# Optimization experiments

Hardware: AMD Instinct MI355X
Metric: run time of the kernel (lower is better)

## Reference

```python
import jax, jax.numpy as jnp
import numpy as np
import math

B, S, D, H = 1, 4096, 1024, 16
DH = D // H


def setup_inputs() -> dict:
    key = jax.random.key(0)
    k1, k2, k3 = jax.random.split(key, 3)
    x = jax.random.normal(k1, (B, S, D), dtype=jnp.float32)
    # additive causal mask: 0 where allowed, -1e9 where masked (future)
    causal = jnp.tril(jnp.ones((S, S), dtype=bool))
    mask = jnp.where(causal, 0.0, -1e9).astype(jnp.float32)[None]  # [1,S,S]
    W_attn = jax.random.normal(k2, (D, 3 * D), dtype=jnp.float32) * 0.02
    b_attn = jnp.zeros((3 * D,), dtype=jnp.float32)
    W_proj = jax.random.normal(k3, (D, D), dtype=jnp.float32) * 0.02
    b_proj = jnp.zeros((D,), dtype=jnp.float32)
    return {"x": x, "mask": mask, "W_attn": W_attn, "b_attn": b_attn,
            "W_proj": W_proj, "b_proj": b_proj}


def reference(x, mask, W_attn, b_attn, W_proj, b_proj):
    # c_attn: fused QKV projection
    qkv = x @ W_attn + b_attn                      # [B,S,3D]
    q, k, v = jnp.split(qkv, 3, axis=-1)           # each [B,S,D]

    def heads(t):  # [B,S,D] -> [B,H,S,DH]
        return t.reshape(B, S, H, DH).transpose(0, 2, 1, 3)

    q, k, v = heads(q), heads(k), heads(v)
    # scores: eager O(S^2) matrix as in original
    w = jnp.einsum('bhqd,bhkd->bhqk', q, k) / math.sqrt(DH)
    w = w + mask[:, None, :, :]                    # broadcast over heads
    w = jax.nn.softmax(w, axis=-1)                 # dropout p=0 -> identity
    a = jnp.einsum('bhqk,bhkd->bhqd', w, v)        # [B,H,S,DH]
    a = a.transpose(0, 2, 1, 3).reshape(B, S, D)   # merge heads
    return a @ W_proj + b_proj
```

## Files before the change

### kernel.cpp

```cpp
#include <hip/hip_runtime.h>

typedef _Float16 half8 __attribute__((ext_vector_type(8)));
typedef short short8 __attribute__((ext_vector_type(8)));
typedef float floatx4 __attribute__((ext_vector_type(4)));

static __device__ __forceinline__ float bf2f(unsigned short u) {
  union { unsigned int u; float f; } c; c.u = ((unsigned int)u) << 16; return c.f;
}
static __device__ __forceinline__ unsigned short f2bf(float f) {
  union { float f; unsigned int u; } c; c.f = f;
  return (unsigned short)((c.u + 0x7fffu + ((c.u >> 16) & 1u)) >> 16);
}

#define GL2LDS16(gsrc, ldst)                                                        \
  __builtin_amdgcn_global_load_lds(                                                 \
      (const __attribute__((address_space(1))) void*)(const void*)(gsrc),           \
      (__attribute__((address_space(3))) void*)(void*)(ldst), 16, 0, 0)

static __device__ __forceinline__ int dtype_bf16(const unsigned short* mask16) {
  return mask16[1] != 0;
}

__global__ __launch_bounds__(256) void k_prep(const void* __restrict__ x,
    const void* __restrict__ Wa, const void* __restrict__ Wp,
    const unsigned short* __restrict__ mask16, _Float16* __restrict__ xh,
    _Float16* __restrict__ WaT, _Float16* __restrict__ WpT) {
  __shared__ float tile[32][33];
  const int dt = dtype_bf16(mask16);
  const int bx = blockIdx.x;
  if (bx < 4096) {
    const int i = (bx * 256 + threadIdx.x) * 4;
    _Float16 o[4];
    if (dt) {
      ushort4 u = *((const ushort4*)((const unsigned short*)x + i));
      o[0] = (_Float16)bf2f(u.x); o[1] = (_Float16)bf2f(u.y);
      o[2] = (_Float16)bf2f(u.z); o[3] = (_Float16)bf2f(u.w);
    } else {
      float4 f = *((const float4*)((const float*)x + i));
      o[0] = (_Float16)f.x; o[1] = (_Float16)f.y;
      o[2] = (_Float16)f.z; o[3] = (_Float16)f.w;
    }
    union { _Float16 h[4]; uint2 u; } pk;
    pk.h[0] = o[0]; pk.h[1] = o[1]; pk.h[2] = o[2]; pk.h[3] = o[3];
    *((uint2*)(xh + i)) = pk.u;
    return;
  }
  const void* in; _Float16* out; int n0, k0;
  if (bx < 7168) { const int b = bx - 4096; in = Wa; out = WaT;
                   n0 = (b % 96) * 32; k0 = (b / 96) * 32;
    const int N = 3072, tid = threadIdx.x, c = tid & 31, r0 = tid >> 5;
#pragma unroll
    for (int i = 0; i < 4; ++i) {
      const int r = r0 + i * 8;
      const size_t src = (size_t)(k0 + r) * N + (n0 + c);
      tile[r][c] = dt ? bf2f(((const unsigned short*)in)[src]) : ((const float*)in)[src];
    }
  } else { const int b = bx - 7168; in = Wp; out = WpT;
           n0 = (b % 32) * 32; k0 = (b / 32) * 32;
    const int N = 1024, tid = threadIdx.x, c = tid & 31, r0 = tid >> 5;
#pragma unroll
    for (int i = 0; i < 4; ++i) {
      const int r = r0 + i * 8;
      const size_t src = (size_t)(k0 + r) * N + (n0 + c);
      tile[r][c] = dt ? bf2f(((const unsigned short*)in)[src]) : ((const float*)in)[src];
    }
  }
  __syncthreads();
  const int tid = threadIdx.x, c = tid & 31, r0 = tid >> 5;
#pragma unroll
  for (int i = 0; i < 4; ++i) {
    const int rr = r0 + i * 8;
    out[(size_t)(n0 + rr) * 1024 + (k0 + c)] = (_Float16)tile[c][rr];
  }
}

template <int KD>
static __device__ __forceinline__ void gemm_mainloop(const _Float16* __restrict__ A,
    const _Float16* __restrict__ Bt, int m0, int n0,
    _Float16* As, _Float16* Bs, floatx4 acc[4][4]) {
  const int tid = threadIdx.x;
  const int wave = tid >> 6, lane = tid & 63;
  const int lq = lane & 15, quad = lane >> 4;
  const int wm = (wave >> 1) * 64, wn = (wave & 1) * 64;
  const int scol = (lane & 3) * 8;
  for (int k0 = 0; k0 < KD; k0 += 32) {
    __syncthreads();
#pragma unroll
    for (int op = 0; op < 2; ++op) {
      const int rbase = wave * 32 + op * 16;
      const int row = rbase + (lane >> 2);
      GL2LDS16(A + (size_t)(m0 + row) * KD + k0 + scol, As + rbase * 32);
      GL2LDS16(Bt + (size_t)(n0 + row) * KD + k0 + scol, Bs + rbase * 32);
    }
    __builtin_amdgcn_s_waitcnt(0x0f70);
    __syncthreads();
    half8 af[4], bf[4];
#pragma unroll
    for (int i = 0; i < 4; ++i) {
      af[i] = *(const half8*)(As + (wm + i * 16 + lq) * 32 + quad * 8);
      bf[i] = *(const half8*)(Bs + (wn + i * 16 + lq) * 32 + quad * 8);
    }
#pragma unroll
    for (int i = 0; i < 4; ++i)
#pragma unroll
      for (int j = 0; j < 4; ++j)
        acc[i][j] = __builtin_amdgcn_mfma_f32_16x16x32_f16(af[i], bf[j], acc[i][j], 0, 0, 0);
  }
}

__global__ __launch_bounds__(256, 1) void k_gemm_qkv(const _Float16* __restrict__ A,
    const _Float16* __restrict__ Bt, const void* __restrict__ bias,
    const unsigned short* __restrict__ mask16, _Float16* __restrict__ Qb,
    _Float16* __restrict__ Kb, unsigned short* __restrict__ VTb) {
  __shared__ __attribute__((aligned(16))) _Float16 As[128 * 32];
  __shared__ __attribute__((aligned(16))) _Float16 Bs[128 * 32];
  const int tid = threadIdx.x, wave = tid >> 6, lane = tid & 63;
  const int lq = lane & 15, quad = lane >> 4;
  const int m0 = blockIdx.y * 128, n0 = blockIdx.x * 128;
  const int wm = (wave >> 1) * 64, wn = (wave & 1) * 64;
  floatx4 acc[4][4] = {};
  gemm_mainloop<1024>(A, Bt, m0, n0, As, Bs, acc);
  const int dt = dtype_bf16(mask16);
  const int sec = n0 >> 10;
  const float scale = (sec == 0) ? 0.1803368801f : 1.0f;
#pragma unroll
  for (int i = 0; i < 4; ++i) {
    const int growb = m0 + wm + i * 16 + quad * 4;
#pragma unroll
    for (int j = 0; j < 4; ++j) {
      const int gcol = n0 + wn + j * 16 + lq;
      const int c = gcol & 1023, hh = c >> 6, dh = c & 63;
      const float bv = dt ? bf2f(((const unsigned short*)bias)[gcol])
                          : ((const float*)bias)[gcol];
      if (sec == 2) {
        union { unsigned short u[4]; uint2 v; } pk;
#pragma unroll
        for (int r = 0; r < 4; ++r) pk.u[r] = f2bf(acc[i][j][r] + bv);
        *(uint2*)(VTb + (size_t)(hh * 64 + dh) * 4096 + growb) = pk.v;
      } else {
        _Float16* dst = (sec == 0) ? Qb : Kb;
#pragma unroll
        for (int r = 0; r < 4; ++r)
          dst[(size_t)(hh * 4096 + growb + r) * 64 + dh] =
              (_Float16)((acc[i][j][r] + bv) * scale);
      }
    }
  }
}

__global__ __launch_bounds__(256, 3) void k_attn(const _Float16* __restrict__ Qb,
    const _Float16* __restrict__ Kb, const unsigned short* __restrict__ VTb,
    unsigned short* __restrict__ Op0, unsigned short* __restrict__ Op1,
    float* __restrict__ Lp) {
  constexpr int S = 4096;
  const int bx = blockIdx.x;
  const int half = bx >> 9;
  const int i5 = bx & 511;
  const int h = i5 & 15;
  const int idx = i5 >> 4;
  const int qb = half ? idx : (31 - idx);
  const int q0 = qb * 128;
  const int t0 = half * (qb + 1);
  const int t1 = t0 + qb + 1;
  const int tid = threadIdx.x, wave = tid >> 6, lane = tid & 63;
  const int lq = lane & 15, quad = lane >> 4;
  __shared__ __attribute__((aligned(16))) _Float16 Ks[64 * 72];
  __shared__ __attribute__((aligned(16))) unsigned short VTs[64 * 72];
  __shared__ __attribute__((aligned(16))) unsigned short Ps[4][32 * 72];
  const _Float16* Qh = Qb + (size_t)h * S * 64;
  const _Float16* Kh = Kb + (size_t)h * S * 64;
  const unsigned short* VTh = VTb + (size_t)h * 64 * S;
  const int qw = q0 + wave * 32;
  half8 qf[2][2];
#pragma unroll
  for (int m = 0; m < 2; ++m)
#pragma unroll
    for (int c = 0; c < 2; ++c)
      qf[m][c] = *(const half8*)(Qh + (size_t)(qw + m * 16 + lq) * 64 + c * 32 + quad * 8);
  short8 aones;
#pragma unroll
  for (int jj = 0; jj < 8; ++jj) aones[jj] = (short)0x3F80;
  floatx4 o[4][2] = {};
  floatx4 ol[2] = {};
  const int srow = tid >> 2, schunk = (tid & 3) * 16;
  uint4 kreg0, kreg1, vreg0, vreg1;
  {
    const int kt = t0 * 64;
    kreg0 = *(const uint4*)(Kh + (size_t)(kt + srow) * 64 + schunk);
    kreg1 = *(const uint4*)(Kh + (size_t)(kt + srow) * 64 + schunk + 8);
    vreg0 = *(const uint4*)(VTh + (size_t)srow * S + kt + schunk);
    vreg1 = *(const uint4*)(VTh + (size_t)srow * S + kt + schunk + 8);
  }
  unsigned short* Pw = &Ps[wave][0];
  for (int t = t0; t < t1; ++t) {
    const int kt = t * 64;
    __syncthreads();
    *(uint4*)(Ks + srow * 72 + schunk) = kreg0;
    *(uint4*)(Ks + srow * 72 + schunk + 8) = kreg1;
    *(uint4*)(VTs + srow * 72 + schunk) = vreg0;
    *(uint4*)(VTs + srow * 72 + schunk + 8) = vreg1;
    __syncthreads();
    if (t + 1 < t1) {
      const int kn = kt + 64;
      kreg0 = *(const uint4*)(Kh + (size_t)(kn + srow) * 64 + schunk);
      kreg1 = *(const uint4*)(Kh + (size_t)(kn + srow) * 64 + schunk + 8);
      vreg0 = *(const uint4*)(VTh + (size_t)srow * S + kn + schunk);
      vreg1 = *(const uint4*)(VTh + (size_t)srow * S + kn + schunk + 8);
    }
    floatx4 sc[2][4];
    {
      half8 kf0[4], kf1[4];
#pragma unroll
      for (int nf = 0; nf < 4; ++nf) {
        kf0[nf] = *(const half8*)(Ks + (nf * 16 + lq) * 72 + quad * 8);
        kf1[nf] = *(const half8*)(Ks + (nf * 16 + lq) * 72 + 32 + quad * 8);
      }
#pragma unroll
      for (int m = 0; m < 2; ++m)
#pragma unroll
        for (int nf = 0; nf < 4; ++nf) {
          floatx4 z = {0.f, 0.f, 0.f, 0.f};
          z = __builtin_amdgcn_mfma_f32_16x16x32_f16(kf0[nf], qf[m][0], z, 0, 0, 0);
          sc[m][nf] = __builtin_amdgcn_mfma_f32_16x16x32_f16(kf1[nf], qf[m][1], z, 0, 0, 0);
        }
    }
#pragma unroll
    for (int m = 0; m < 2; ++m) {
      const int q = qw + m * 16 + lq;
      if (kt + 63 > qw + m * 16) {
#pragma unroll
        for (int nf = 0; nf < 4; ++nf) {
          const int key = kt + nf * 16 + quad * 4;
          float p[4];
#pragma unroll
          for (int r = 0; r < 4; ++r) {
            float e = __builtin_amdgcn_exp2f(sc[m][nf][r]);
            p[r] = (key + r > q) ? 0.f : e;
          }
          uint2 pk;
          pk.x = __builtin_amdgcn_perm(__float_as_uint(p[1]), __float_as_uint(p[0]),
                                       0x07060302u);
          pk.y = __builtin_amdgcn_perm(__float_as_uint(p[3]), __float_as_uint(p[2]),
                                       0x07060302u);
          *(uint2*)(Pw + (m * 16 + lq) * 72 + nf * 16 + quad * 4) = pk;
        }
      } else {
#pragma unroll
        for (int nf = 0; nf < 4; ++nf) {
          float p[4];
#pragma unroll
          for (int r = 0; r < 4; ++r) p[r] = __builtin_amdgcn_exp2f(sc[m][nf][r]);
          uint2 pk;
          pk.x = __builtin_amdgcn_perm(__float_as_uint(p[1]), __float_as_uint(p[0]),
                                       0x07060302u);
          pk.y = __builtin_amdgcn_perm(__float_as_uint(p[3]), __float_as_uint(p[2]),
                                       0x07060302u);
          *(uint2*)(Pw + (m * 16 + lq) * 72 + nf * 16 + quad * 4) = pk;
        }
      }
    }
    __builtin_amdgcn_s_waitcnt(0xC07F);
#pragma unroll
    for (int c = 0; c < 2; ++c) {
      short8 pf[2];
#pragma unroll
      for (int m = 0; m < 2; ++m)
        pf[m] = *(const short8*)(Pw + (m * 16 + lq) * 72 + c * 32 + quad * 8);
#pragma unroll
      for (int nf = 0; nf < 4; ++nf) {
        const short8 vfr = *(const short8*)(VTs + (nf * 16 + lq) * 72 + c * 32 + quad * 8);
#pragma unroll
        for (int m = 0; m < 2; ++m)
          o[nf][m] = __builtin_amdgcn_mfma_f32_16x16x32_bf16(vfr, pf[m], o[nf][m], 0, 0, 0);
      }
#pragma unroll
      for (int m = 0; m < 2; ++m)
        ol[m] = __builtin_amdgcn_mfma_f32_16x16x32_bf16(aones, pf[m], ol[m], 0, 0, 0);
    }
  }
  unsigned short* Op = half ? Op1 : Op0;
#pragma unroll
  for (int m = 0; m < 2; ++m) {
    const int q = qw + m * 16 + lq;
#pragma unroll
    for (int nf = 0; nf < 4; ++nf) {
      union { unsigned short u[4]; uint2 v; } pk;
#pragma unroll
      for (int r = 0; r < 4; ++r) pk.u[r] = f2bf(o[nf][m][r]);
      *(uint2*)(Op + (size_t)q * 1024 + h * 64 + nf * 16 + quad * 4) = pk.v;
    }
    if (quad == 0) Lp[half * 65536 + h * 4096 + q] = ol[m][0];
  }
}

__global__ __launch_bounds__(256) void k_merge(const unsigned short* __restrict__ Op0,
    const unsigned short* __restrict__ Op1, const float* __restrict__ Lp,
    _Float16* __restrict__ Ah) {
  const int row = blockIdx.x;
  const int c = threadIdx.x * 4;
  const int h = c >> 6;
  const float l = Lp[h * 4096 + row] + Lp[65536 + h * 4096 + row];
  const float inv = __builtin_amdgcn_rcpf(l);
  const size_t idx = (size_t)row * 1024 + c;
  const ushort4 a = *(const ushort4*)(Op0 + idx);
  const ushort4 b = *(const ushort4*)(Op1 + idx);
  union { _Float16 h4[4]; uint2 u; } pk;
  pk.h4[0] = (_Float16)((bf2f(a.x) + bf2f(b.x)) * inv);
  pk.h4[1] = (_Float16)((bf2f(a.y) + bf2f(b.y)) * inv);
  pk.h4[2] = (_Float16)((bf2f(a.z) + bf2f(b.z)) * inv);
  pk.h4[3] = (_Float16)((bf2f(a.w) + bf2f(b.w)) * inv);
  *(uint2*)(Ah + idx) = pk.u;
}

__global__ __launch_bounds__(256, 1) void k_gemm_proj(const _Float16* __restrict__ A,
    const _Float16* __restrict__ Bt, const void* __restrict__ bias,
    const unsigned short* __restrict__ mask16, void* __restrict__ out) {
  __shared__ __attribute__((aligned(16))) _Float16 As[128 * 32];
  __shared__ __attribute__((aligned(16))) _Float16 Bs[128 * 32];
  const int tid = threadIdx.x, wave = tid >> 6, lane = tid & 63;
  const int lq = lane & 15, quad = lane >> 4;
  const int m0 = blockIdx.y * 128, n0 = blockIdx.x * 128;
  const int wm = (wave >> 1) * 64, wn = (wave & 1) * 64;
  floatx4 acc[4][4] = {};
  gemm_mainloop<1024>(A, Bt, m0, n0, As, Bs, acc);
  const int dt = dtype_bf16(mask16);
#pragma unroll
  for (int i = 0; i < 4; ++i) {
    const int growb = m0 + wm + i * 16 + quad * 4;
#pragma unroll
    for (int j = 0; j < 4; ++j) {
      const int gcol = n0 + wn + j * 16 + lq;
      const float bv = dt ? bf2f(((const unsigned short*)bias)[gcol])
                          : ((const float*)bias)[gcol];
#pragma unroll
      for (int r = 0; r < 4; ++r) {
        const float v = acc[i][j][r] + bv;
        if (dt) ((unsigned short*)out)[(size_t)(growb + r) * 1024 + gcol] = f2bf(v);
        else    ((float*)out)[(size_t)(growb + r) * 1024 + gcol] = v;
      }
    }
  }
}

extern "C" void kernel_launch(void* const* d_in, const int* in_sizes, int n_in,
                              void* d_out, int out_size, void* d_ws, size_t ws_size,
                              hipStream_t stream) {
  const void* x    = d_in[0];
  const unsigned short* mask16 = (const unsigned short*)d_in[1];
  const void* Wa   = d_in[2];
  const void* ba   = d_in[3];
  const void* Wp   = d_in[4];
  const void* bp   = d_in[5];
  char* ws = (char*)d_ws;
  _Float16* WpT       = (_Float16*)(ws + 0);
  _Float16* WaT       = (_Float16*)(ws + 2097152);
  float*    Lp        = (float*)   (ws + 2097152);
  _Float16* xh        = (_Float16*)(ws + 8388608);
  unsigned short* Op0 = (unsigned short*)(ws + 8388608);
  _Float16* Qb        = (_Float16*)(ws + 16777216);
  _Float16* Kb        = (_Float16*)(ws + 25165824);
  unsigned short* VTb = (unsigned short*)(ws + 33554432);
  _Float16* Ah        = (_Float16*)(ws + 41943040);
  unsigned short* Op1 = (unsigned short*)(ws + 41943040);

  k_prep<<<8192, 256, 0, stream>>>(x, Wa, Wp, mask16, xh, WaT, WpT);
  { dim3 g(24, 32); k_gemm_qkv<<<g, 256, 0, stream>>>(xh, WaT, ba, mask16, Qb, Kb, VTb); }
  k_attn<<<1024, 256, 0, stream>>>(Qb, Kb, VTb, Op0, Op1, Lp);
  k_merge<<<4096, 256, 0, stream>>>(Op0, Op1, Lp, Ah);
  { dim3 g(8, 32);  k_gemm_proj<<<g, 256, 0, stream>>>(Ah, WpT, bp, mask16, d_out); }
}
```

Measured before the change: 269.9 us.

## Vectorize weight transpose, stage QKV epilogue through LDS, halve proj GEMM tile

The weight transpose in prep now uses 64x64 tiles with vectorized loads and 4-wide packed stores instead of scalar 32x32 tiles. The QKV GEMM epilogue writes results into shared memory first and then emits coalesced 16-byte stores for Q, K and transposed V, replacing scattered 2-byte global stores. The projection GEMM switches to 64x128 tiles so the grid doubles to 512 blocks and fills more CUs. The costs are extra LDS usage and syncs in the QKV epilogue, and lower MFMA reuse per block in the projection GEMM.

```diff
diff --git a/kernel.cpp b/kernel.cpp
--- a/kernel.cpp
+++ b/kernel.cpp
@@ -10,6 +10,9 @@
 static __device__ __forceinline__ unsigned short f2bf(float f) {
   union { float f; unsigned int u; } c; c.f = f;
   return (unsigned short)((c.u + 0x7fffu + ((c.u >> 16) & 1u)) >> 16);
+}
+static __device__ __forceinline__ unsigned short f2h(float f) {
+  union { _Float16 h; unsigned short u; } c; c.h = (_Float16)f; return c.u;
 }
 
 #define GL2LDS16(gsrc, ldst)                                                        \
@@ -25,11 +28,12 @@
     const void* __restrict__ Wa, const void* __restrict__ Wp,
     const unsigned short* __restrict__ mask16, _Float16* __restrict__ xh,
     _Float16* __restrict__ WaT, _Float16* __restrict__ WpT) {
-  __shared__ float tile[32][33];
+  __shared__ float tile[64 * 65];
   const int dt = dtype_bf16(mask16);
   const int bx = blockIdx.x;
+  const int tid = threadIdx.x;
   if (bx < 4096) {
-    const int i = (bx * 256 + threadIdx.x) * 4;
+    const int i = (bx * 256 + tid) * 4;
     _Float16 o[4];
     if (dt) {
       ushort4 u = *((const ushort4*)((const unsigned short*)x + i));
@@ -45,32 +49,37 @@
     *((uint2*)(xh + i)) = pk.u;
     return;
   }
-  const void* in; _Float16* out; int n0, k0;
-  if (bx < 7168) { const int b = bx - 4096; in = Wa; out = WaT;
-                   n0 = (b % 96) * 32; k0 = (b / 96) * 32;
-    const int N = 3072, tid = threadIdx.x, c = tid & 31, r0 = tid >> 5;
-#pragma unroll
-    for (int i = 0; i < 4; ++i) {
-      const int r = r0 + i * 8;
-      const size_t src = (size_t)(k0 + r) * N + (n0 + c);
-      tile[r][c] = dt ? bf2f(((const unsigned short*)in)[src]) : ((const float*)in)[src];
-    }
-  } else { const int b = bx - 7168; in = Wp; out = WpT;
-           n0 = (b % 32) * 32; k0 = (b / 32) * 32;
-    const int N = 1024, tid = threadIdx.x, c = tid & 31, r0 = tid >> 5;
-#pragma unroll
-    for (int i = 0; i < 4; ++i) {
-      const int r = r0 + i * 8;
-      const size_t src = (size_t)(k0 + r) * N + (n0 + c);
-      tile[r][c] = dt ? bf2f(((const unsigned short*)in)[src]) : ((const float*)in)[src];
-    }
+  const void* in; _Float16* out; int n0, k0, N;
+  if (bx < 4864) { const int b = bx - 4096; in = Wa; out = WaT; N = 3072;
+                   n0 = (b % 48) * 64; k0 = (b / 48) * 64; }
+  else           { const int b = bx - 4864; in = Wp; out = WpT; N = 1024;
+                   n0 = (b % 16) * 64; k0 = (b / 16) * 64; }
+  const int r = tid >> 2;
+#pragma unroll
+  for (int it = 0; it < 4; ++it) {
+    const int c4 = (tid & 3) + it * 4;
+    const size_t src = (size_t)(k0 + r) * N + n0 + c4 * 4;
+    float v[4];
+    if (dt) {
+      ushort4 u = *((const ushort4*)((const unsigned short*)in + src));
+      v[0] = bf2f(u.x); v[1] = bf2f(u.y); v[2] = bf2f(u.z); v[3] = bf2f(u.w);
+    } else {
+      float4 f = *((const float4*)((const float*)in + src));
+      v[0] = f.x; v[1] = f.y; v[2] = f.z; v[3] = f.w;
+    }
+#pragma unroll
+    for (int jj = 0; jj < 4; ++jj) tile[r * 65 + c4 * 4 + jj] = v[jj];
   }
   __syncthreads();
-  const int tid = threadIdx.x, c = tid & 31, r0 = tid >> 5;
-#pragma unroll
-  for (int i = 0; i < 4; ++i) {
-    const int rr = r0 + i * 8;
-    out[(size_t)(n0 + rr) * 1024 + (k0 + c)] = (_Float16)tile[c][rr];
+#pragma unroll
+  for (int it = 0; it < 4; ++it) {
+    const int rn = (tid >> 4) + it * 16;
+    const int kc = tid & 15;
+    union { _Float16 h[4]; uint2 u; } pk;
+#pragma unroll
+    for (int jj = 0; jj < 4; ++jj)
+      pk.h[jj] = (_Float16)tile[(kc * 4 + jj) * 65 + rn];
+    *(uint2*)(out + (size_t)(n0 + rn) * 1024 + k0 + kc * 4) = pk.u;
   }
 }
 
@@ -112,8 +121,9 @@
     const _Float16* __restrict__ Bt, const void* __restrict__ bias,
     const unsigned short* __restrict__ mask16, _Float16* __restrict__ Qb,
     _Float16* __restrict__ Kb, unsigned short* __restrict__ VTb) {
-  __shared__ __attribute__((aligned(16))) _Float16 As[128 * 32];
-  __shared__ __attribute__((aligned(16))) _Float16 Bs[128 * 32];
+  __shared__ __attribute__((aligned(16))) unsigned short smem[128 * 136];
+  _Float16* As = (_Float16*)smem;
+  _Float16* Bs = As + 4096;
   const int tid = threadIdx.x, wave = tid >> 6, lane = tid & 63;
   const int lq = lane & 15, quad = lane >> 4;
   const int m0 = blockIdx.y * 128, n0 = blockIdx.x * 128;
@@ -123,27 +133,44 @@
   const int dt = dtype_bf16(mask16);
   const int sec = n0 >> 10;
   const float scale = (sec == 0) ? 0.1803368801f : 1.0f;
+  __syncthreads();
 #pragma unroll
   for (int i = 0; i < 4; ++i) {
-    const int growb = m0 + wm + i * 16 + quad * 4;
+    const int lmb = wm + i * 16 + quad * 4;
 #pragma unroll
     for (int j = 0; j < 4; ++j) {
-      const int gcol = n0 + wn + j * 16 + lq;
-      const int c = gcol & 1023, hh = c >> 6, dh = c & 63;
+      const int ln = wn + j * 16 + lq;
+      const int gcol = n0 + ln;
       const float bv = dt ? bf2f(((const unsigned short*)bias)[gcol])
                           : ((const float*)bias)[gcol];
-      if (sec == 2) {
-        union { unsigned short u[4]; uint2 v; } pk;
-#pragma unroll
-        for (int r = 0; r < 4; ++r) pk.u[r] = f2bf(acc[i][j][r] + bv);
-        *(uint2*)(VTb + (size_t)(hh * 64 + dh) * 4096 + growb) = pk.v;
-      } else {
-        _Float16* dst = (sec == 0) ? Qb : Kb;
-#pragma unroll
-        for (int r = 0; r < 4; ++r)
-          dst[(size_t)(hh * 4096 + growb + r) * 64 + dh] =
-              (_Float16)((acc[i][j][r] + bv) * scale);
-      }
+#pragma unroll
+      for (int r = 0; r < 4; ++r) {
+        const float v = (acc[i][j][r] + bv) * scale;
+        const unsigned short bits = (sec == 2) ? f2bf(v) : f2h(v);
+        if (sec == 2) smem[ln * 136 + lmb + r] = bits;
+        else          smem[(lmb + r) * 136 + ln] = bits;
+      }
+    }
+  }
+  __syncthreads();
+  if (sec == 2) {
+#pragma unroll
+    for (int it = 0; it < 8; ++it) {
+      const int row = (tid >> 4) + it * 16;
+      const int ch = tid & 15;
+      const uint4 v = *(const uint4*)&smem[row * 136 + ch * 8];
+      *(uint4*)(VTb + (size_t)(n0 + row - 2048) * 4096 + m0 + ch * 8) = v;
+    }
+  } else {
+    _Float16* dst = (sec == 0) ? Qb : Kb;
+#pragma unroll
+    for (int it = 0; it < 8; ++it) {
+      const int row = (tid >> 4) + it * 16;
+      const int ch = tid & 15;
+      const uint4 v = *(const uint4*)&smem[row * 136 + ch * 8];
+      const int c = (n0 & 1023) + ch * 8;
+      const int hh = c >> 6, dh = c & 63;
+      *(uint4*)(dst + ((size_t)(hh * 4096 + m0 + row)) * 64 + dh) = v;
     }
   }
 }
@@ -315,17 +342,44 @@
 __global__ __launch_bounds__(256, 1) void k_gemm_proj(const _Float16* __restrict__ A,
     const _Float16* __restrict__ Bt, const void* __restrict__ bias,
     const unsigned short* __restrict__ mask16, void* __restrict__ out) {
-  __shared__ __attribute__((aligned(16))) _Float16 As[128 * 32];
+  __shared__ __attribute__((aligned(16))) _Float16 As[64 * 32];
   __shared__ __attribute__((aligned(16))) _Float16 Bs[128 * 32];
   const int tid = threadIdx.x, wave = tid >> 6, lane = tid & 63;
   const int lq = lane & 15, quad = lane >> 4;
-  const int m0 = blockIdx.y * 128, n0 = blockIdx.x * 128;
-  const int wm = (wave >> 1) * 64, wn = (wave & 1) * 64;
-  floatx4 acc[4][4] = {};
-  gemm_mainloop<1024>(A, Bt, m0, n0, As, Bs, acc);
+  const int m0 = blockIdx.y * 64, n0 = blockIdx.x * 128;
+  const int wm = (wave >> 1) * 32, wn = (wave & 1) * 64;
+  const int scol = (lane & 3) * 8;
+  floatx4 acc[2][4] = {};
+  for (int k0 = 0; k0 < 1024; k0 += 32) {
+    __syncthreads();
+    {
+      const int arow = wave * 16 + (lane >> 2);
+      GL2LDS16(A + (size_t)(m0 + arow) * 1024 + k0 + scol, As + wave * 16 * 32);
+#pragma unroll
+      for (int op = 0; op < 2; ++op) {
+        const int rbase = wave * 32 + op * 16;
+        const int row = rbase + (lane >> 2);
+        GL2LDS16(Bt + (size_t)(n0 + row) * 1024 + k0 + scol, Bs + rbase * 32);
+      }
+    }
+    __builtin_amdgcn_s_waitcnt(0x0f70);
+    __syncthreads();
+    half8 af[2], bf[4];
+#pragma unroll
+    for (int i = 0; i < 2; ++i)
+      af[i] = *(const half8*)(As + (wm + i * 16 + lq) * 32 + quad * 8);
+#pragma unroll
+    for (int j = 0; j < 4; ++j)
+      bf[j] = *(const half8*)(Bs + (wn + j * 16 + lq) * 32 + quad * 8);
+#pragma unroll
+    for (int i = 0; i < 2; ++i)
+#pragma unroll
+      for (int j = 0; j < 4; ++j)
+        acc[i][j] = __builtin_amdgcn_mfma_f32_16x16x32_f16(af[i], bf[j], acc[i][j], 0, 0, 0);
+  }
   const int dt = dtype_bf16(mask16);
 #pragma unroll
-  for (int i = 0; i < 4; ++i) {
+  for (int i = 0; i < 2; ++i) {
     const int growb = m0 + wm + i * 16 + quad * 4;
 #pragma unroll
     for (int j = 0; j < 4; ++j) {
@@ -363,9 +417,9 @@
   _Float16* Ah        = (_Float16*)(ws + 41943040);
   unsigned short* Op1 = (unsigned short*)(ws + 41943040);
 
-  k_prep<<<8192, 256, 0, stream>>>(x, Wa, Wp, mask16, xh, WaT, WpT);
+  k_prep<<<5120, 256, 0, stream>>>(x, Wa, Wp, mask16, xh, WaT, WpT);
   { dim3 g(24, 32); k_gemm_qkv<<<g, 256, 0, stream>>>(xh, WaT, ba, mask16, Qb, Kb, VTb); }
   k_attn<<<1024, 256, 0, stream>>>(Qb, Kb, VTb, Op0, Op1, Lp);
   k_merge<<<4096, 256, 0, stream>>>(Op0, Op1, Lp, Ah);
-  { dim3 g(8, 32);  k_gemm_proj<<<g, 256, 0, stream>>>(Ah, WpT, bp, mask16, d_out); }
-}
+  { dim3 g(8, 64);  k_gemm_proj<<<g, 256, 0, stream>>>(Ah, WpT, bp, mask16, d_out); }
+}
```

Result: faster. 252.1 us (-6.6%).
